# Performance work log

Measured on AMD Instinct MI355X. Metric: run time of the kernel, lower is better.

## Reference

```python
import jax, jax.numpy as jnp
import numpy as np

B = 16
NT, NH_, NW_, T_, H_, W_ = 4, 14, 14, 4, 1, 1
C = 768
NHEAD = 12
HD = C // NHEAD
SCALE = 1.0 / float(np.sqrt(HD))
TT = NT * T_            # 16 temporal slices
T2 = TT // 2            # 8 after even/odd split
HW = (NH_ * H_) * (NW_ * W_)  # 196 spatial tokens
TOKENS = NT * NH_ * NW_ * T_ * H_ * W_


def setup_inputs() -> dict:
    key = jax.random.key(0)
    ks = jax.random.split(key, 14)
    def lin(k, din, dout):
        return jax.random.normal(k, (din, dout), jnp.float32) * 0.02
    return {
        "x_in": jax.random.normal(ks[0], (B, TOKENS, C), jnp.float32),
        "Wq_d": lin(ks[1], C, C),      "bq_d": jnp.zeros((C,), jnp.float32),
        "Wkv_a": lin(ks[2], C, 2 * C), "bkv_a": jnp.zeros((2 * C,), jnp.float32),
        "Wq_a": lin(ks[3], C, C),      "bq_a": jnp.zeros((C,), jnp.float32),
        "Wkv_d": lin(ks[4], C, 2 * C), "bkv_d": jnp.zeros((2 * C,), jnp.float32),
        "Wp_d": lin(ks[5], C, C),      "bp_d": jnp.zeros((C,), jnp.float32),
        "Wp_a": lin(ks[6], C, C),      "bp_a": jnp.zeros((C,), jnp.float32),
    }


def _cross_attn(q_x, kv_x, Wq, bq, Wkv, bkv):
    # q_x, kv_x: (b, t, hw, c)
    b, t, hw, c = q_x.shape
    q = (q_x @ Wq + bq).reshape(b, t, hw, NHEAD, HD)
    kv = (kv_x @ Wkv + bkv).reshape(b, t, hw, 2, NHEAD, HD)
    k, v = kv[..., 0, :, :], kv[..., 1, :, :]
    s = jnp.einsum('btqhd,btkhd->bthqk', q, k) * SCALE
    p = jax.nn.softmax(s, axis=-1)
    o = jnp.einsum('bthqk,btkhd->btqhd', p, v)
    return o.reshape(b, t, hw, c)


def reference(x_in, Wq_d, bq_d, Wkv_a, bkv_a, Wq_a, bq_a, Wkv_d, bkv_d,
              Wp_d, bp_d, Wp_a, bp_a):
    b = x_in.shape[0]
    # einops: b (nt nh nw t h w) c -> b (nt t) (nh h) (nw w) c
    x = x_in.reshape(b, NT, NH_, NW_, T_, H_, W_, C)
    x = x.transpose(0, 1, 4, 2, 5, 3, 6, 7).reshape(b, TT, NH_ * H_, NW_ * W_, C)
    x_skip = x                                   # (b, TT, h, w, c)
    x = x.reshape(b, TT, HW, C)                  # (b, TT, hw, c)
    x_a = x[:, 0::2]                             # (b, T2, hw, c) approx
    x_d = x[:, 1::2]                             # (b, T2, hw, c) detail

    # detail cross-attends to approx, subtract-update
    _d = _cross_attn(x_d, x_a, Wq_d, bq_d, Wkv_a, bkv_a)
    _d = jax.nn.gelu(_d @ Wp_d + bp_d, approximate=False)
    x_d = x_d - _d
    # approx cross-attends to updated detail, add-update
    _a = _cross_attn(x_a, x_d, Wq_a, bq_a, Wkv_d, bkv_d)
    _a = jax.nn.gelu(_a @ Wp_a + bp_a, approximate=False)
    x_a = x_a + _a

    # relaxed_constrain: pooled-skip minus channel-mean of x_a
    xs = x_skip.reshape(b, TT, HW, C)
    pooled = xs.reshape(b, T2, 2, HW, C).mean(axis=2)   # avg_pool2d (2,1)
    pool_a = pooled.mean(axis=-1) - x_a.mean(axis=-1)   # (b, T2, hw)

    # SSL=False: mean over channels, keepdim (torch layout b,1,t,hw)
    x_d_out = x_d.mean(axis=-1)[:, None, :, :]          # (b, 1, T2, hw)
    return (pool_a, x_d_out)
```

## Files before the change

kernel.cpp:

```cpp
#include <hip/hip_runtime.h>

typedef __bf16 bf16;
typedef __attribute__((ext_vector_type(8))) __bf16 bf16x8;
typedef __attribute__((ext_vector_type(4))) __bf16 bf16x4;
typedef __attribute__((ext_vector_type(2))) __bf16 bf16x2;
typedef __attribute__((ext_vector_type(4))) float f32x4;
typedef __attribute__((ext_vector_type(4))) unsigned int u32x4;

#define TOKENS 3136
#define CC 768
#define S196 196
#define M_ROWS 25088
#define BATCH 16

__device__ __forceinline__ float bf2f(bf16 x) { return (float)x; }
__device__ __forceinline__ bf16 f2bf(float x) { return (bf16)x; }

__device__ __forceinline__ float gelu_exact(float x) {
    return 0.5f * x * (1.0f + erff(x * 0.70710678118654752f));
}

__device__ __forceinline__ unsigned int packbf(float a, float b) {
    bf16x2 v; v[0] = (bf16)a; v[1] = (bf16)b;
    return __builtin_bit_cast(unsigned int, v);
}

#define GLOAD_LDS16(gp, lp) \
    __builtin_amdgcn_global_load_lds((const __attribute__((address_space(1))) void*)(gp), \
                                     (__attribute__((address_space(3))) void*)(lp), 16, 0, 0)

__global__ __launch_bounds__(256)
void transpose_w(const float* __restrict__ W, bf16* __restrict__ Wt, int K, int N)
{
    __shared__ float tle[32][33];
    int k0 = blockIdx.x * 32, n0 = blockIdx.y * 32;
    int tx = threadIdx.x & 31, ty = threadIdx.x >> 5;
    for (int r = ty; r < 32; r += 8)
        tle[r][tx] = W[(long)(k0 + r) * N + n0 + tx];
    __syncthreads();
    for (int r = ty; r < 32; r += 8)
        Wt[(long)(n0 + r) * K + k0 + tx] = f2bf(tle[tx][r]);
}

__global__ __launch_bounds__(256)
void conv_bias(const float* b0, const float* b1, const float* b2,
               const float* b3, const float* b4, const float* b5,
               bf16* __restrict__ dst)
{
    const float* srcs[6] = {b0, b1, b2, b3, b4, b5};
    const int sizes[6]   = {768, 1536, 768, 1536, 768, 768};
    const int offs[6]    = {0, 768, 2304, 3072, 4608, 5376};
    int which = blockIdx.x;
    const float* s = srcs[which];
    int n = sizes[which];
    bf16* d = dst + offs[which];
    for (int i = threadIdx.x; i < n; i += 256)
        d[i] = f2bf(s[i]);
}

__global__ __launch_bounds__(256)
void reorder_split(const float* __restrict__ x_in, bf16* __restrict__ xa,
                   bf16* __restrict__ xd)
{
    long idx = (long)blockIdx.x * 256 + threadIdx.x;
    const long total = (long)BATCH * 16 * S196 * 96;
    if (idx >= total) return;
    int  c8  = (int)(idx % 96) * 8;
    long row = idx / 96;
    int  s   = (int)(row % S196);
    long r2  = row / S196;
    int  tt  = (int)(r2 & 15);
    int  b   = (int)(r2 >> 4);
    int  nt  = tt >> 2, t = tt & 3;
    int  nh  = s / 14,  nw = s % 14;
    long src  = ((long)b * TOKENS + ((nt * 14 + nh) * 14 + nw) * 4 + t) * CC + c8;
    bf16* dst = (tt & 1) ? xd : xa;
    long doff = ((long)(b * 8 + (tt >> 1)) * S196 + s) * CC + c8;
    const float* sp = x_in + src;
    f32x4 a = *(const f32x4*)sp;
    f32x4 c = *(const f32x4*)(sp + 4);
    bf16x8 v;
    v[0] = f2bf(a[0]); v[1] = f2bf(a[1]); v[2] = f2bf(a[2]); v[3] = f2bf(a[3]);
    v[4] = f2bf(c[0]); v[5] = f2bf(c[1]); v[6] = f2bf(c[2]); v[7] = f2bf(c[3]);
    *(bf16x8*)(dst + doff) = v;
}

__device__ __forceinline__ float row_sum768(const bf16* __restrict__ p, int lane)
{
    float s = 0.f;
    bf16x8 v = *(const bf16x8*)(p + lane * 8);
    #pragma unroll
    for (int j = 0; j < 8; ++j) s += bf2f(v[j]);
    if (lane < 32) {
        bf16x8 w = *(const bf16x8*)(p + 512 + lane * 8);
        #pragma unroll
        for (int j = 0; j < 8; ++j) s += bf2f(w[j]);
    }
    #pragma unroll
    for (int off = 32; off; off >>= 1) s += __shfl_xor(s, off, 64);
    return s;
}

__global__ __launch_bounds__(256)
void pool_ad(const bf16* __restrict__ xa, const bf16* __restrict__ xd,
             float* __restrict__ pool0)
{
    int id = blockIdx.x * 4 + (threadIdx.x >> 6);
    int lane = threadIdx.x & 63;
    float sa = row_sum768(xa + (long)id * CC, lane);
    float sd = row_sum768(xd + (long)id * CC, lane);
    if (lane == 0) pool0[id] = (sa + sd) * (0.5f / 768.0f);
}

__global__ __launch_bounds__(256)
void out_final(const bf16* __restrict__ xa, const bf16* __restrict__ xd,
               const float* __restrict__ pool0, float* __restrict__ out)
{
    int id = blockIdx.x * 4 + (threadIdx.x >> 6);
    int lane = threadIdx.x & 63;
    float sa = row_sum768(xa + (long)id * CC, lane);
    float sd = row_sum768(xd + (long)id * CC, lane);
    if (lane == 0) {
        out[id]          = pool0[id] - sa * (1.0f / 768.0f);
        out[M_ROWS + id] = sd * (1.0f / 768.0f);
    }
}

template<int EPI>
__global__ __launch_bounds__(256)
void gemm_bt(const bf16* __restrict__ A, const bf16* __restrict__ Bt,
             const bf16* __restrict__ bias, const bf16* __restrict__ res,
             bf16* __restrict__ C, int ldc, int K, int mTiles, int nTiles)
{
    constexpr int BM = 128, BK = 32;
    __shared__ alignas(16) bf16 sA[BM * BK];
    __shared__ alignas(16) bf16 sB[BM * BK];
    const int tid  = threadIdx.x;
    const int lane = tid & 63, wave = tid >> 6;
    const int wm   = wave >> 1, wn = wave & 1;
    const int quad = lane >> 4, l16 = lane & 15;

    const int GM = 16;
    int pid   = blockIdx.x;
    int group = GM * nTiles;
    int gid   = pid / group;
    int rem   = pid - gid * group;
    int first = gid * GM;
    int gm    = (mTiles - first < GM) ? (mTiles - first) : GM;
    int bm    = first + rem % gm;
    int bn    = rem / gm;

    const long m0 = (long)bm * BM;
    const long n0 = (long)bn * BM;

    f32x4 acc[4][4] = {};

    for (int kt = 0; kt < K; kt += BK) {
        if (kt) __syncthreads();
        #pragma unroll
        for (int c = 0; c < 2; ++c) {
            int ci = (wave * 2 + c) * 64 + lane;
            int r  = ci >> 2, kc = ci & 3;
            const bf16* ga = A  + (m0 + r) * K + kt + kc * 8;
            const bf16* gb = Bt + (n0 + r) * K + kt + kc * 8;
            bf16* la = sA + (wave * 2 + c) * 512;
            bf16* lb = sB + (wave * 2 + c) * 512;
            GLOAD_LDS16(ga, la);
            GLOAD_LDS16(gb, lb);
        }
        __syncthreads();

        bf16x8 af[4], bfr[4];
        #pragma unroll
        for (int mi = 0; mi < 4; ++mi)
            af[mi] = *(const bf16x8*)(sA + (wm * 64 + mi * 16 + l16) * BK + quad * 8);
        #pragma unroll
        for (int ni = 0; ni < 4; ++ni)
            bfr[ni] = *(const bf16x8*)(sB + (wn * 64 + ni * 16 + l16) * BK + quad * 8);
        #pragma unroll
        for (int mi = 0; mi < 4; ++mi)
            #pragma unroll
            for (int ni = 0; ni < 4; ++ni)
                acc[mi][ni] = __builtin_amdgcn_mfma_f32_16x16x32_bf16(af[mi], bfr[ni], acc[mi][ni], 0, 0, 0);
    }

    #pragma unroll
    for (int mi = 0; mi < 4; ++mi) {
        #pragma unroll
        for (int ni = 0; ni < 4; ++ni) {
            int mg = (int)m0 + wm * 64 + mi * 16 + quad * 4;
            int ng = (int)n0 + wn * 64 + ni * 16 + l16;
            float bn_ = bf2f(bias[ng]);
            #pragma unroll
            for (int r = 0; r < 4; ++r) {
                float x = acc[mi][ni][r] + bn_;
                long off = (long)(mg + r) * ldc + ng;
                if (EPI == 0)      C[off] = f2bf(x);
                else if (EPI == 1) C[off] = f2bf(bf2f(res[off]) - gelu_exact(x));
                else               C[off] = f2bf(bf2f(res[off]) + gelu_exact(x));
            }
        }
    }
}

#define KSTR 72
#define VSTR 264

__global__ __launch_bounds__(256)
void attn_mfma(const bf16* __restrict__ Q, int ldq,
               const bf16* __restrict__ KV, int ldkv,
               bf16* __restrict__ O)
{
    const int h  = blockIdx.x;
    const int bj = blockIdx.y;
    __shared__ alignas(16) bf16 Ks[208 * KSTR];
    __shared__ alignas(16) bf16 Vt[64 * VSTR];
    const int tid = threadIdx.x, lane = tid & 63, wave = tid >> 6;
    const int quad = lane >> 4, l16 = lane & 15;

    const bf16* qg = Q  + (long)bj * S196 * ldq  + h * 64;
    const bf16* kg = KV + (long)bj * S196 * ldkv + h * 64;
    const bf16* vg = kg + CC;

    for (int i = tid; i < 208 * 8; i += 256) {
        int r = i >> 3, c8 = (i & 7) * 8;
        bf16x8 v = {};
        if (r < S196) v = *(const bf16x8*)(kg + (long)r * ldkv + c8);
        *(bf16x8*)(Ks + r * KSTR + c8) = v;
    }
    for (int i = tid; i < 256 * 8; i += 256) {
        int g   = i >> 6;
        int c8  = (g & 7) * 8;
        int tok = (g >> 3) * 64 + (i & 63);
        bf16x8 v = {};
        if (tok < S196) v = *(const bf16x8*)(vg + (long)tok * ldkv + c8);
        #pragma unroll
        for (int j = 0; j < 8; ++j)
            Vt[(c8 + j) * VSTR + tok] = v[j];
    }
    __syncthreads();

    for (int qt = wave; qt < 13; qt += 4) {
        int qrow = qt * 16 + l16; if (qrow > 195) qrow = 195;
        const bf16* qrp = qg + (long)qrow * ldq + quad * 8;
        bf16x8 qf0 = *(const bf16x8*)(qrp);
        bf16x8 qf1 = *(const bf16x8*)(qrp + 32);

        f32x4 st[13];
        #pragma unroll
        for (int rt = 0; rt < 13; ++rt) st[rt] = (f32x4){0.f, 0.f, 0.f, 0.f};
        #pragma unroll
        for (int rt = 0; rt < 13; ++rt) {
            const bf16* kb = Ks + (rt * 16 + l16) * KSTR + quad * 8;
            bf16x8 kf0 = *(const bf16x8*)(kb);
            bf16x8 kf1 = *(const bf16x8*)(kb + 32);
            st[rt] = __builtin_amdgcn_mfma_f32_16x16x32_bf16(kf0, qf0, st[rt], 0, 0, 0);
            st[rt] = __builtin_amdgcn_mfma_f32_16x16x32_bf16(kf1, qf1, st[rt], 0, 0, 0);
        }

        const float SC = 0.125f;
        #pragma unroll
        for (int rt = 0; rt < 13; ++rt) {
            st[rt][0] *= SC; st[rt][1] *= SC; st[rt][2] *= SC; st[rt][3] *= SC;
        }
        if (quad != 0)
            st[12] = (f32x4){-1e30f, -1e30f, -1e30f, -1e30f};

        float m = -1e30f;
        #pragma unroll
        for (int rt = 0; rt < 13; ++rt)
            m = fmaxf(m, fmaxf(fmaxf(st[rt][0], st[rt][1]), fmaxf(st[rt][2], st[rt][3])));
        m = fmaxf(m, __shfl_xor(m, 16, 64));
        m = fmaxf(m, __shfl_xor(m, 32, 64));
        float sum = 0.f;
        #pragma unroll
        for (int rt = 0; rt < 13; ++rt) {
            st[rt][0] = __expf(st[rt][0] - m);
            st[rt][1] = __expf(st[rt][1] - m);
            st[rt][2] = __expf(st[rt][2] - m);
            st[rt][3] = __expf(st[rt][3] - m);
            sum += st[rt][0] + st[rt][1] + st[rt][2] + st[rt][3];
        }
        sum += __shfl_xor(sum, 16, 64);
        sum += __shfl_xor(sum, 32, 64);
        float inv = 1.0f / sum;

        unsigned int pk[13][2];
        #pragma unroll
        for (int rt = 0; rt < 13; ++rt) {
            pk[rt][0] = packbf(st[rt][0] * inv, st[rt][1] * inv);
            pk[rt][1] = packbf(st[rt][2] * inv, st[rt][3] * inv);
        }

        f32x4 ot[4];
        #pragma unroll
        for (int dt = 0; dt < 4; ++dt) ot[dt] = (f32x4){0.f, 0.f, 0.f, 0.f};
        #pragma unroll
        for (int c = 0; c < 7; ++c) {
            u32x4 fp;
            #pragma unroll
            for (int jp = 0; jp < 4; ++jp) {
                int jh = jp >> 1, rp = jp & 1;
                int srcb = ((((quad & 1) << 1) + jh) << 6) | (l16 << 2);
                int a = __builtin_amdgcn_ds_bpermute(srcb, (int)pk[2 * c][rp]);
                int b = (c < 6) ? __builtin_amdgcn_ds_bpermute(srcb, (int)pk[2 * c + 1][rp]) : 0;
                fp[jp] = (quad >> 1) ? (unsigned int)b : (unsigned int)a;
            }
            bf16x8 pB = __builtin_bit_cast(bf16x8, fp);
            #pragma unroll
            for (int dt = 0; dt < 4; ++dt) {
                bf16x8 vf = *(const bf16x8*)(Vt + (dt * 16 + l16) * VSTR + c * 32 + quad * 8);
                ot[dt] = __builtin_amdgcn_mfma_f32_16x16x32_bf16(vf, pB, ot[dt], 0, 0, 0);
            }
        }

        int token = qt * 16 + l16;
        if (token < S196) {
            bf16* op = O + ((long)bj * S196 + token) * CC + h * 64 + quad * 4;
            #pragma unroll
            for (int dt = 0; dt < 4; ++dt) {
                bf16x4 v;
                v[0] = f2bf(ot[dt][0]); v[1] = f2bf(ot[dt][1]);
                v[2] = f2bf(ot[dt][2]); v[3] = f2bf(ot[dt][3]);
                *(bf16x4*)(op + dt * 16) = v;
            }
        }
    }
}

extern "C" void kernel_launch(void* const* d_in, const int* in_sizes, int n_in,
                              void* d_out, int out_size, void* d_ws, size_t ws_size,
                              hipStream_t stream)
{
    const float* x_in  = (const float*)d_in[0];
    const float* Wq_d  = (const float*)d_in[1];
    const float* bq_d  = (const float*)d_in[2];
    const float* Wkv_a = (const float*)d_in[3];
    const float* bkv_a = (const float*)d_in[4];
    const float* Wq_a  = (const float*)d_in[5];
    const float* bq_a  = (const float*)d_in[6];
    const float* Wkv_d = (const float*)d_in[7];
    const float* bkv_d = (const float*)d_in[8];
    const float* Wp_d  = (const float*)d_in[9];
    const float* bp_d  = (const float*)d_in[10];
    const float* Wp_a  = (const float*)d_in[11];
    const float* bp_a  = (const float*)d_in[12];
    float* out = (float*)d_out;

    char* w = (char*)d_ws;
    auto alloc = [&](size_t elems) {
        bf16* p = (bf16*)w;
        w += ((elems * 2 + 255) / 256) * 256;
        return p;
    };
    bf16* biasAll = alloc(6144);
    bf16* WtQd  = alloc((size_t)768 * 768);
    bf16* WtACat= alloc((size_t)2304 * 768);
    bf16* WtKd  = alloc((size_t)1536 * 768);
    bf16* WtPd  = alloc((size_t)768 * 768);
    bf16* WtPa  = alloc((size_t)768 * 768);
    bf16* xa    = alloc((size_t)M_ROWS * 768);
    bf16* xd    = alloc((size_t)M_ROWS * 768);
    bf16* Qb    = alloc((size_t)M_ROWS * 768);
    bf16* QKVa  = alloc((size_t)M_ROWS * 2304);
    bf16* Ob    = alloc((size_t)M_ROWS * 768);
    float* pool0 = (float*)w; w += ((size_t)M_ROWS * 4 + 255) / 256 * 256;

    dim3 blk(256);
    transpose_w<<<dim3(24, 24), blk, 0, stream>>>(Wq_d,  WtQd, 768, 768);
    transpose_w<<<dim3(24, 48), blk, 0, stream>>>(Wkv_a, WtACat, 768, 1536);
    transpose_w<<<dim3(24, 24), blk, 0, stream>>>(Wq_a,  WtACat + (size_t)1536 * 768, 768, 768);
    transpose_w<<<dim3(24, 48), blk, 0, stream>>>(Wkv_d, WtKd, 768, 1536);
    transpose_w<<<dim3(24, 24), blk, 0, stream>>>(Wp_d,  WtPd, 768, 768);
    transpose_w<<<dim3(24, 24), blk, 0, stream>>>(Wp_a,  WtPa, 768, 768);
    conv_bias<<<dim3(6), blk, 0, stream>>>(bq_d, bkv_a, bq_a, bkv_d, bp_d, bp_a, biasAll);

    long total_chunks = (long)BATCH * 16 * S196 * 96;
    int  rblocks = (int)((total_chunks + 255) / 256);
    reorder_split<<<rblocks, blk, 0, stream>>>(x_in, xa, xd);
    pool_ad<<<M_ROWS / 4, blk, 0, stream>>>(xa, xd, pool0);

    const bf16* Bq_d   = biasAll;
    const bf16* Bkva_qa= biasAll + 768;
    const bf16* Bkv_d  = biasAll + 3072;
    const bf16* Bp_d   = biasAll + 4608;
    const bf16* Bp_a   = biasAll + 5376;

    gemm_bt<0><<<196 * 6,  blk, 0, stream>>>(xd, WtQd,  Bq_d,    nullptr, Qb,   768,  768, 196, 6);
    gemm_bt<0><<<196 * 18, blk, 0, stream>>>(xa, WtACat, Bkva_qa, nullptr, QKVa, 2304, 768, 196, 18);
    attn_mfma<<<dim3(12, 128), blk, 0, stream>>>(Qb, 768, QKVa, 2304, Ob);
    gemm_bt<1><<<196 * 6,  blk, 0, stream>>>(Ob, WtPd, Bp_d, xd, xd, 768, 768, 196, 6);

    gemm_bt<0><<<196 * 12, blk, 0, stream>>>(xd, WtKd, Bkv_d, nullptr, QKVa, 2304, 768, 196, 12);
    attn_mfma<<<dim3(12, 128), blk, 0, stream>>>(QKVa + 1536, 2304, QKVa, 2304, Ob);
    gemm_bt<2><<<196 * 6,  blk, 0, stream>>>(Ob, WtPa, Bp_a, xa, xa, 768, 768, 196, 6);

    out_final<<<M_ROWS / 4, blk, 0, stream>>>(xa, xd, pool0, out);
}
```

Measured before the change: 873.8 us.

## Enlarge GEMM tiles with triple-buffered async LDS pipeline and swizzled layout

Reworks the bf16 GEMM to use 256x128x64 tiles on 512-thread blocks, with a three-stage buffer of global-to-LDS loads issued two k-steps ahead. Loads are split across the two compute halves, and waits use vmcnt counting instead of a full barrier every iteration. LDS rows get an XOR swizzle to avoid bank conflicts, and MFMA sections raise wave priority. This aims to hide memory latency and raise operand reuse, at the cost of about 147KB of LDS, one block per CU, and a coarser grid.

```diff
diff --git a/kernel.cpp b/kernel.cpp
--- a/kernel.cpp
+++ b/kernel.cpp
@@ -127,14 +127,14 @@
 }
 
 template<int EPI>
-__global__ __launch_bounds__(256)
+__global__ __launch_bounds__(512, 1)
 void gemm_bt(const bf16* __restrict__ A, const bf16* __restrict__ Bt,
              const bf16* __restrict__ bias, const bf16* __restrict__ res,
              bf16* __restrict__ C, int ldc, int K, int mTiles, int nTiles)
 {
-    constexpr int BM = 128, BK = 32;
-    __shared__ alignas(16) bf16 sA[BM * BK];
-    __shared__ alignas(16) bf16 sB[BM * BK];
+    constexpr int BM = 256, BN = 128, BK = 64, NBUF = 3;
+    __shared__ alignas(16) bf16 sA[NBUF][BM * BK];
+    __shared__ alignas(16) bf16 sB[NBUF][BN * BK];
     const int tid  = threadIdx.x;
     const int lane = tid & 63, wave = tid >> 6;
     const int wm   = wave >> 1, wn = wave & 1;
@@ -151,38 +151,74 @@
     int bn    = rem / gm;
 
     const long m0 = (long)bm * BM;
-    const long n0 = (long)bn * BM;
+    const long n0 = (long)bn * BN;
+    const int  NKT = K / BK;
+
+    const int rsub = lane >> 3;
+    const int clog = (lane & 7) ^ rsub;
 
     f32x4 acc[4][4] = {};
 
-    for (int kt = 0; kt < K; kt += BK) {
-        if (kt) __syncthreads();
-        #pragma unroll
-        for (int c = 0; c < 2; ++c) {
-            int ci = (wave * 2 + c) * 64 + lane;
-            int r  = ci >> 2, kc = ci & 3;
-            const bf16* ga = A  + (m0 + r) * K + kt + kc * 8;
-            const bf16* gb = Bt + (n0 + r) * K + kt + kc * 8;
-            bf16* la = sA + (wave * 2 + c) * 512;
-            bf16* lb = sB + (wave * 2 + c) * 512;
-            GLOAD_LDS16(ga, la);
-            GLOAD_LDS16(gb, lb);
-        }
-        __syncthreads();
-
+    #define STAGE_A(buf, kt2, j) do { \
+        int q_ = (j) * 8 + wave; \
+        const bf16* g_ = A + (m0 + q_ * 8 + rsub) * (long)K + (kt2) * BK + clog * 8; \
+        GLOAD_LDS16(g_, &sA[buf][q_ * 512]); } while (0)
+    #define STAGE_B(buf, kt2, j) do { \
+        int q_ = (j) * 8 + wave; \
+        const bf16* g_ = Bt + (n0 + q_ * 8 + rsub) * (long)K + (kt2) * BK + clog * 8; \
+        GLOAD_LDS16(g_, &sB[buf][q_ * 512]); } while (0)
+
+    STAGE_A(0, 0, 0); STAGE_A(0, 0, 1); STAGE_A(0, 0, 2); STAGE_A(0, 0, 3);
+    STAGE_B(0, 0, 0); STAGE_B(0, 0, 1);
+    STAGE_A(1, 1, 0); STAGE_A(1, 1, 1); STAGE_A(1, 1, 2); STAGE_A(1, 1, 3);
+    STAGE_B(1, 1, 0); STAGE_B(1, 1, 1);
+    asm volatile("s_waitcnt vmcnt(6)" ::: "memory");
+    __builtin_amdgcn_s_barrier();
+
+    auto compute = [&](int buf, int kk) {
         bf16x8 af[4], bfr[4];
         #pragma unroll
-        for (int mi = 0; mi < 4; ++mi)
-            af[mi] = *(const bf16x8*)(sA + (wm * 64 + mi * 16 + l16) * BK + quad * 8);
-        #pragma unroll
-        for (int ni = 0; ni < 4; ++ni)
-            bfr[ni] = *(const bf16x8*)(sB + (wn * 64 + ni * 16 + l16) * BK + quad * 8);
+        for (int mi = 0; mi < 4; ++mi) {
+            int ra = wm * 64 + mi * 16 + l16;
+            int cs = (kk * 4 + quad) ^ (ra & 7);
+            af[mi] = *(const bf16x8*)(&sA[buf][ra * 64 + cs * 8]);
+        }
+        #pragma unroll
+        for (int ni = 0; ni < 4; ++ni) {
+            int rb = wn * 64 + ni * 16 + l16;
+            int cs = (kk * 4 + quad) ^ (rb & 7);
+            bfr[ni] = *(const bf16x8*)(&sB[buf][rb * 64 + cs * 8]);
+        }
+        __builtin_amdgcn_s_setprio(1);
         #pragma unroll
         for (int mi = 0; mi < 4; ++mi)
             #pragma unroll
             for (int ni = 0; ni < 4; ++ni)
                 acc[mi][ni] = __builtin_amdgcn_mfma_f32_16x16x32_bf16(af[mi], bfr[ni], acc[mi][ni], 0, 0, 0);
-    }
+        __builtin_amdgcn_s_setprio(0);
+    };
+
+    int cur = 0;
+    for (int kt = 0; kt < NKT; ++kt) {
+        int nxt2 = cur + 2; if (nxt2 >= NBUF) nxt2 -= NBUF;
+        const bool doStage = (kt + 2 < NKT);
+
+        if (doStage) { STAGE_A(nxt2, kt + 2, 0); STAGE_A(nxt2, kt + 2, 1); STAGE_B(nxt2, kt + 2, 0); }
+        compute(cur, 0);
+        if (doStage) { STAGE_A(nxt2, kt + 2, 2); STAGE_A(nxt2, kt + 2, 3); STAGE_B(nxt2, kt + 2, 1); }
+        compute(cur, 1);
+
+        if (kt + 2 < NKT) {
+            asm volatile("s_waitcnt vmcnt(6)" ::: "memory");
+            __builtin_amdgcn_s_barrier();
+        } else if (kt + 1 < NKT) {
+            asm volatile("s_waitcnt vmcnt(0)" ::: "memory");
+            __builtin_amdgcn_s_barrier();
+        }
+        cur = cur + 1; if (cur == NBUF) cur = 0;
+    }
+    #undef STAGE_A
+    #undef STAGE_B
 
     #pragma unroll
     for (int mi = 0; mi < 4; ++mi) {
@@ -367,6 +403,7 @@
     float* pool0 = (float*)w; w += ((size_t)M_ROWS * 4 + 255) / 256 * 256;
 
     dim3 blk(256);
+    dim3 blk512(512);
     transpose_w<<<dim3(24, 24), blk, 0, stream>>>(Wq_d,  WtQd, 768, 768);
     transpose_w<<<dim3(24, 48), blk, 0, stream>>>(Wkv_a, WtACat, 768, 1536);
     transpose_w<<<dim3(24, 24), blk, 0, stream>>>(Wq_a,  WtACat + (size_t)1536 * 768, 768, 768);
@@ -386,14 +423,14 @@
     const bf16* Bp_d   = biasAll + 4608;
     const bf16* Bp_a   = biasAll + 5376;
 
-    gemm_bt<0><<<196 * 6,  blk, 0, stream>>>(xd, WtQd,  Bq_d,    nullptr, Qb,   768,  768, 196, 6);
-    gemm_bt<0><<<196 * 18, blk, 0, stream>>>(xa, WtACat, Bkva_qa, nullptr, QKVa, 2304, 768, 196, 18);
+    gemm_bt<0><<<dim3(98 * 6),  blk512, 0, stream>>>(xd, WtQd,  Bq_d,    nullptr, Qb,   768,  768, 98, 6);
+    gemm_bt<0><<<dim3(98 * 18), blk512, 0, stream>>>(xa, WtACat, Bkva_qa, nullptr, QKVa, 2304, 768, 98, 18);
     attn_mfma<<<dim3(12, 128), blk, 0, stream>>>(Qb, 768, QKVa, 2304, Ob);
-    gemm_bt<1><<<196 * 6,  blk, 0, stream>>>(Ob, WtPd, Bp_d, xd, xd, 768, 768, 196, 6);
-
-    gemm_bt<0><<<196 * 12, blk, 0, stream>>>(xd, WtKd, Bkv_d, nullptr, QKVa, 2304, 768, 196, 12);
+    gemm_bt<1><<<dim3(98 * 6),  blk512, 0, stream>>>(Ob, WtPd, Bp_d, xd, xd, 768, 768, 98, 6);
+
+    gemm_bt<0><<<dim3(98 * 12), blk512, 0, stream>>>(xd, WtKd, Bkv_d, nullptr, QKVa, 2304, 768, 98, 12);
     attn_mfma<<<dim3(12, 128), blk, 0, stream>>>(QKVa + 1536, 2304, QKVa, 2304, Ob);
-    gemm_bt<2><<<196 * 6,  blk, 0, stream>>>(Ob, WtPa, Bp_a, xa, xa, 768, 768, 196, 6);
+    gemm_bt<2><<<dim3(98 * 6),  blk512, 0, stream>>>(Ob, WtPa, Bp_a, xa, xa, 768, 768, 98, 6);
 
     out_final<<<M_ROWS / 4, blk, 0, stream>>>(xa, xd, pool0, out);
 }
```

New measurement: 951.3 us. 8.9% more time.

## Rewrite GEMM as 256x256 tile, 512-thread, multi-stage pipelined kernel with swizzled LDS

Applied to the files above, without the earlier changes.

Replaces the 128x128 single-buffer GEMM with a 256x256 tile computed by 8 waves. It uses a 4-slot LDS ring fed by direct global-to-LDS loads, XOR-swizzled LDS addressing, and interleaved barriers with wave priority raised around the MFMA bursts. The aim is to hide global load latency behind MFMA work, raise arithmetic intensity per tile, and avoid LDS bank conflicts. K is hardcoded to 768 and the grids are relaunched with 512-thread blocks. The larger tiles mean fewer blocks per GEMM (294 to 882), which risks tail and occupancy effects.

```diff
diff --git a/kernel.cpp b/kernel.cpp
--- a/kernel.cpp
+++ b/kernel.cpp
@@ -127,20 +127,20 @@
 }
 
 template<int EPI>
-__global__ __launch_bounds__(256)
+__global__ __launch_bounds__(512, 2)
 void gemm_bt(const bf16* __restrict__ A, const bf16* __restrict__ Bt,
              const bf16* __restrict__ bias, const bf16* __restrict__ res,
-             bf16* __restrict__ C, int ldc, int K, int mTiles, int nTiles)
-{
-    constexpr int BM = 128, BK = 32;
-    __shared__ alignas(16) bf16 sA[BM * BK];
-    __shared__ alignas(16) bf16 sB[BM * BK];
+             bf16* __restrict__ C, int ldc, int mTiles, int nTiles)
+{
+    constexpr int K = 768, NKT = 12;
+    __shared__ alignas(16) bf16 sA[4][8192];
+    __shared__ alignas(16) bf16 sB[4][8192];
     const int tid  = threadIdx.x;
     const int lane = tid & 63, wave = tid >> 6;
-    const int wm   = wave >> 1, wn = wave & 1;
+    const int wm   = wave >> 2, wn = wave & 3;
     const int quad = lane >> 4, l16 = lane & 15;
 
-    const int GM = 16;
+    const int GM = 8;
     int pid   = blockIdx.x;
     int group = GM * nTiles;
     int gid   = pid / group;
@@ -150,50 +150,108 @@
     int bm    = first + rem % gm;
     int bn    = rem / gm;
 
-    const long m0 = (long)bm * BM;
-    const long n0 = (long)bn * BM;
-
-    f32x4 acc[4][4] = {};
-
-    for (int kt = 0; kt < K; kt += BK) {
-        if (kt) __syncthreads();
-        #pragma unroll
-        for (int c = 0; c < 2; ++c) {
-            int ci = (wave * 2 + c) * 64 + lane;
-            int r  = ci >> 2, kc = ci & 3;
-            const bf16* ga = A  + (m0 + r) * K + kt + kc * 8;
-            const bf16* gb = Bt + (n0 + r) * K + kt + kc * 8;
-            bf16* la = sA + (wave * 2 + c) * 512;
-            bf16* lb = sB + (wave * 2 + c) * 512;
-            GLOAD_LDS16(ga, la);
-            GLOAD_LDS16(gb, lb);
-        }
-        __syncthreads();
-
-        bf16x8 af[4], bfr[4];
-        #pragma unroll
-        for (int mi = 0; mi < 4; ++mi)
-            af[mi] = *(const bf16x8*)(sA + (wm * 64 + mi * 16 + l16) * BK + quad * 8);
-        #pragma unroll
-        for (int ni = 0; ni < 4; ++ni)
-            bfr[ni] = *(const bf16x8*)(sB + (wn * 64 + ni * 16 + l16) * BK + quad * 8);
-        #pragma unroll
-        for (int mi = 0; mi < 4; ++mi)
-            #pragma unroll
-            for (int ni = 0; ni < 4; ++ni)
-                acc[mi][ni] = __builtin_amdgcn_mfma_f32_16x16x32_bf16(af[mi], bfr[ni], acc[mi][ni], 0, 0, 0);
-    }
+    const long m0 = (long)bm * 256;
+    const long n0 = (long)bn * 256;
+
+    const int fl    = (l16 & 3) ^ (l16 >> 2);
+    const int aoffA = (wm * 128 + l16) * 32 + ((quad ^ fl) * 8);
+    const int aoffB = (wn * 64  + l16) * 32 + ((quad ^ fl) * 8);
+
+    const int  cch = (lane & 3) ^ ((lane >> 2) & 3) ^ quad;
+    const int  r0  = wave * 16 + (lane >> 2);
+    const int  r1  = (8 + wave) * 16 + (lane >> 2);
+    const long so0 = (long)r0 * K + cch * 8;
+    const long so1 = (long)r1 * K + cch * 8;
+    const int  ld0 = wave * 512, ld1 = (8 + wave) * 512;
+    const bf16* Ab = A  + m0 * K;
+    const bf16* Bb = Bt + n0 * K;
+
+    f32x4 acc[8][4] = {};
+
+    #define STG_A(slot, koff) do { \
+        GLOAD_LDS16(Ab + (koff) + so0, &sA[slot][ld0]); \
+        GLOAD_LDS16(Ab + (koff) + so1, &sA[slot][ld1]); } while (0)
+    #define STG_B(slot, koff) do { \
+        GLOAD_LDS16(Bb + (koff) + so0, &sB[slot][ld0]); \
+        GLOAD_LDS16(Bb + (koff) + so1, &sB[slot][ld1]); } while (0)
+
+    STG_A(0, 0);  STG_B(0, 0);
+    STG_A(1, 32); STG_B(1, 32);
+    STG_A(2, 64); STG_B(2, 64);
+    asm volatile("s_waitcnt vmcnt(8)" ::: "memory");
+    __builtin_amdgcn_s_barrier();
+
+    #define MFMA16(H) do { \
+        __builtin_amdgcn_s_setprio(1); \
+        _Pragma("unroll") \
+        for (int mf = 0; mf < 4; ++mf) \
+            _Pragma("unroll") \
+            for (int nf = 0; nf < 4; ++nf) \
+                acc[(H)*4 + mf][nf] = __builtin_amdgcn_mfma_f32_16x16x32_bf16( \
+                    a[mf], b[nf], acc[(H)*4 + mf][nf], 0, 0, 0); \
+        __builtin_amdgcn_s_setprio(0); } while (0)
+
+    #pragma unroll 2
+    for (int t = 0; t < NKT; ++t) {
+        const int sl0 = (2 * t) & 3;
+        const int sl1 = (2 * t + 1) & 3;
+        const int slN = (2 * t + 3) & 3;
+        bf16x8 a[4], b[4];
+
+        #pragma unroll
+        for (int mf = 0; mf < 4; ++mf) a[mf] = *(const bf16x8*)(&sA[sl0][mf * 512 + aoffA]);
+        #pragma unroll
+        for (int nf = 0; nf < 4; ++nf) b[nf] = *(const bf16x8*)(&sB[sl0][nf * 512 + aoffB]);
+        if (t + 1 < NKT) STG_A(slN, (t + 1) * 64 + 32);
+        __builtin_amdgcn_s_barrier();
+        __builtin_amdgcn_sched_barrier(0);
+        MFMA16(0);
+        __builtin_amdgcn_s_barrier();
+
+        #pragma unroll
+        for (int mf = 0; mf < 4; ++mf) a[mf] = *(const bf16x8*)(&sA[sl0][2048 + mf * 512 + aoffA]);
+        if (t + 1 < NKT) STG_B(slN, (t + 1) * 64 + 32);
+        __builtin_amdgcn_s_barrier();
+        __builtin_amdgcn_sched_barrier(0);
+        MFMA16(1);
+        if (t + 1 < NKT) asm volatile("s_waitcnt vmcnt(8)" ::: "memory");
+        else             asm volatile("s_waitcnt vmcnt(0)" ::: "memory");
+        __builtin_amdgcn_s_barrier();
+
+        #pragma unroll
+        for (int mf = 0; mf < 4; ++mf) a[mf] = *(const bf16x8*)(&sA[sl1][mf * 512 + aoffA]);
+        #pragma unroll
+        for (int nf = 0; nf < 4; ++nf) b[nf] = *(const bf16x8*)(&sB[sl1][nf * 512 + aoffB]);
+        if (t + 2 < NKT) STG_A(sl0, (t + 2) * 64);
+        __builtin_amdgcn_s_barrier();
+        __builtin_amdgcn_sched_barrier(0);
+        MFMA16(0);
+        __builtin_amdgcn_s_barrier();
+
+        #pragma unroll
+        for (int mf = 0; mf < 4; ++mf) a[mf] = *(const bf16x8*)(&sA[sl1][2048 + mf * 512 + aoffA]);
+        if (t + 2 < NKT) STG_B(sl0, (t + 2) * 64);
+        __builtin_amdgcn_s_barrier();
+        __builtin_amdgcn_sched_barrier(0);
+        MFMA16(1);
+        if      (t + 2 < NKT) asm volatile("s_waitcnt vmcnt(8)" ::: "memory");
+        else if (t + 1 < NKT) asm volatile("s_waitcnt vmcnt(4)" ::: "memory");
+        __builtin_amdgcn_s_barrier();
+    }
+    #undef STG_A
+    #undef STG_B
+    #undef MFMA16
 
     #pragma unroll
-    for (int mi = 0; mi < 4; ++mi) {
-        #pragma unroll
-        for (int ni = 0; ni < 4; ++ni) {
-            int mg = (int)m0 + wm * 64 + mi * 16 + quad * 4;
-            int ng = (int)n0 + wn * 64 + ni * 16 + l16;
+    for (int mf = 0; mf < 8; ++mf) {
+        #pragma unroll
+        for (int nf = 0; nf < 4; ++nf) {
+            int mg = (int)m0 + wm * 128 + mf * 16 + quad * 4;
+            int ng = (int)n0 + wn * 64 + nf * 16 + l16;
             float bn_ = bf2f(bias[ng]);
             #pragma unroll
             for (int r = 0; r < 4; ++r) {
-                float x = acc[mi][ni][r] + bn_;
+                float x = acc[mf][nf][r] + bn_;
                 long off = (long)(mg + r) * ldc + ng;
                 if (EPI == 0)      C[off] = f2bf(x);
                 else if (EPI == 1) C[off] = f2bf(bf2f(res[off]) - gelu_exact(x));
@@ -367,6 +425,7 @@
     float* pool0 = (float*)w; w += ((size_t)M_ROWS * 4 + 255) / 256 * 256;
 
     dim3 blk(256);
+    dim3 blk512(512);
     transpose_w<<<dim3(24, 24), blk, 0, stream>>>(Wq_d,  WtQd, 768, 768);
     transpose_w<<<dim3(24, 48), blk, 0, stream>>>(Wkv_a, WtACat, 768, 1536);
     transpose_w<<<dim3(24, 24), blk, 0, stream>>>(Wq_a,  WtACat + (size_t)1536 * 768, 768, 768);
@@ -386,14 +445,14 @@
     const bf16* Bp_d   = biasAll + 4608;
     const bf16* Bp_a   = biasAll + 5376;
 
-    gemm_bt<0><<<196 * 6,  blk, 0, stream>>>(xd, WtQd,  Bq_d,    nullptr, Qb,   768,  768, 196, 6);
-    gemm_bt<0><<<196 * 18, blk, 0, stream>>>(xa, WtACat, Bkva_qa, nullptr, QKVa, 2304, 768, 196, 18);
+    gemm_bt<0><<<dim3(98 * 3), blk512, 0, stream>>>(xd, WtQd,  Bq_d,    nullptr, Qb,   768,  98, 3);
+    gemm_bt<0><<<dim3(98 * 9), blk512, 0, stream>>>(xa, WtACat, Bkva_qa, nullptr, QKVa, 2304, 98, 9);
     attn_mfma<<<dim3(12, 128), blk, 0, stream>>>(Qb, 768, QKVa, 2304, Ob);
-    gemm_bt<1><<<196 * 6,  blk, 0, stream>>>(Ob, WtPd, Bp_d, xd, xd, 768, 768, 196, 6);
-
-    gemm_bt<0><<<196 * 12, blk, 0, stream>>>(xd, WtKd, Bkv_d, nullptr, QKVa, 2304, 768, 196, 12);
+    gemm_bt<1><<<dim3(98 * 3), blk512, 0, stream>>>(Ob, WtPd, Bp_d, xd, xd, 768, 98, 3);
+
+    gemm_bt<0><<<dim3(98 * 6), blk512, 0, stream>>>(xd, WtKd, Bkv_d, nullptr, QKVa, 2304, 98, 6);
     attn_mfma<<<dim3(12, 128), blk, 0, stream>>>(QKVa + 1536, 2304, QKVa, 2304, Ob);
-    gemm_bt<2><<<196 * 6,  blk, 0, stream>>>(Ob, WtPa, Bp_a, xa, xa, 768, 768, 196, 6);
+    gemm_bt<2><<<dim3(98 * 3), blk512, 0, stream>>>(Ob, WtPa, Bp_a, xa, xa, 768, 98, 3);
 
     out_final<<<M_ROWS / 4, blk, 0, stream>>>(xa, xd, pool0, out);
 }
```

Measured after the change: 936.8 us. 7.2% more time.
